# Optimization experiments

Measured on AMD Instinct MI355X. Metric: run time of the kernel, lower is better.

The kernel has to match this reference:

```python
import jax, jax.numpy as jnp
import numpy as np

B, D, V, S = 256, 784, 128, 2  # batch, dim, max_val, n_steps
ITER_PER_CYCLE = 10
STEP_SIZES = [0.5] + [0.1] * (ITER_PER_CYCLE - 1)   # sbc: [big_step] + [small_step]*...
BAL_CONSTS = [0.9] + [0.6] * (ITER_PER_CYCLE - 1)   # sbc: [big_bal] + [small_bal]*...
TEMP = 1.0


def setup_inputs() -> dict:
    key = jax.random.key(0)
    k1, k2, k3, k4, k5 = jax.random.split(key, 5)
    x = jax.random.randint(k1, (B, D), 0, V, dtype=jnp.int32)
    W = jax.random.normal(k2, (D, D), dtype=jnp.float32) * (1.0 / D)  # keep energies moderate
    b = jax.random.normal(k3, (D,), dtype=jnp.float32) * 0.1
    # Pre-sampled Gumbel noise for the categorical proposal (one slab per inner step)
    ug = jax.random.uniform(k4, (S, B, D, V), dtype=jnp.float32, minval=1e-6, maxval=1.0 - 1e-6)
    gumbel = -jnp.log(-jnp.log(ug))
    # Uniform draws for the MH accept/reject test
    u = jax.random.uniform(k5, (S, B), dtype=jnp.float32)
    k_iter = 0
    return {"x": x, "W": W, "b": b, "gumbel": gumbel, "u": u, "k_iter": k_iter}


def reference(x, W, b, gumbel, u, k_iter):
    step_size = STEP_SIZES[k_iter % ITER_PER_CYCLE]
    bal = BAL_CONSTS[k_iter % ITER_PER_CYCLE]
    Wsym = 0.5 * (W + W.T)

    def model(xf):                      # energy: [B]
        return 0.5 * jnp.einsum('bi,bi->b', xf, xf @ Wsym) + xf @ b

    def gradf(xf):                      # d(energy)/dx: [B, D]
        return xf @ Wsym + b

    disc = jnp.arange(V, dtype=jnp.float32)[None, None, :]  # [1,1,V]

    def calc_logits(xf, g):
        # term1 - term2 from _calc_logits, fused elementwise over [B, D, V]
        diff = disc - xf[:, :, None]
        return g[:, :, None] * diff * bal - diff * diff * (0.5 / step_size)

    def body(x_cur, inp):
        g_noise, ui = inp
        xf = x_cur.astype(jnp.float32)
        g = gradf(xf)
        logits = calc_logits(xf, g)                                  # [B,D,V]
        x_delta = jnp.argmax(logits + g_noise, axis=-1)              # categorical sample [B,D]
        logp = jax.nn.log_softmax(logits, axis=-1)
        lp_forward = jnp.take_along_axis(logp, x_delta[:, :, None], axis=-1)[..., 0].sum(axis=1)
        xdf = x_delta.astype(jnp.float32)
        gd = gradf(xdf) / TEMP
        logits_d = calc_logits(xdf, gd)
        logp_d = jax.nn.log_softmax(logits_d, axis=-1)
        lp_reverse = jnp.take_along_axis(logp_d, x_cur[:, :, None], axis=-1)[..., 0].sum(axis=1)
        la = model(xdf) - model(xf) + lp_reverse - lp_forward        # log accept ratio [B]
        acc = jnp.exp(la) > ui
        x_new = jnp.where(acc[:, None], x_delta, x_cur).astype(x_cur.dtype)
        return x_new, la

    x_out, las = jax.lax.scan(body, x, (gumbel, u))
    return x_out, las[-1]
```

## Files before the change

kernel.cpp:

```cpp
#include <hip/hip_runtime.h>

#define B_ 256
#define D_ 784
#define V_ 128
#define S_ 2
#define BD (B_ * D_)
#define KSPLIT 8

__device__ __forceinline__ void get_params(const int* kiter, float& ss, float& bal) {
    int k = kiter[0] % 10;
    ss  = (k == 0) ? 0.5f : 0.1f;
    bal = (k == 0) ? 0.9f : 0.6f;
}

__device__ __forceinline__ double wave_red(double v) {
#pragma unroll
    for (int o = 32; o > 0; o >>= 1) v += __shfl_down(v, o, 64);
    return v;
}

__global__ __launch_bounds__(256) void init_k(
    const float* __restrict__ W, const int* __restrict__ x,
    float* __restrict__ wsym, int* __restrict__ x_cur, float* __restrict__ xf)
{
    int gid = blockIdx.x * 256 + threadIdx.x;
    if (gid < D_ * D_) {
        int i = gid / D_, j = gid % D_;
        wsym[gid] = 0.5f * (W[gid] + W[j * D_ + i]);
    }
    if (gid < BD) {
        int xi = x[gid];
        x_cur[gid] = xi;
        xf[gid] = (float)xi;
    }
}

__global__ __launch_bounds__(256) void gemm_splitk(
    const float* __restrict__ A, const float* __restrict__ Wm,
    float* __restrict__ Cp)
{
    const int bt = blockIdx.x, dt = blockIdx.y, kz = blockIdx.z;
    const int tid = threadIdx.x;
    const int k0 = kz * 98, kend = k0 + 98;

    __shared__ float As[64][17];
    __shared__ float Ws[16][65];

    const int tx = tid & 15, ty = tid >> 4;
    const int arow = tid >> 2, ac0 = (tid & 3) * 4;
    const int wrow = tid >> 4, wc0 = (tid & 15) * 4;

    float acc[4][4] = {};

    for (int kb = k0; kb < kend; kb += 16) {
#pragma unroll
        for (int c = 0; c < 4; ++c) {
            int k = kb + ac0 + c;
            As[arow][ac0 + c] = (k < kend) ? A[(bt * 64 + arow) * D_ + k] : 0.f;
        }
#pragma unroll
        for (int c = 0; c < 4; ++c) {
            int k = kb + wrow;
            int d = dt * 64 + wc0 + c;
            Ws[wrow][wc0 + c] = (k < kend && d < D_) ? Wm[k * D_ + d] : 0.f;
        }
        __syncthreads();
#pragma unroll
        for (int kk = 0; kk < 16; ++kk) {
            float a[4], w[4];
#pragma unroll
            for (int i = 0; i < 4; ++i) a[i] = As[ty * 4 + i][kk];
#pragma unroll
            for (int j = 0; j < 4; ++j) w[j] = Ws[kk][tx * 4 + j];
#pragma unroll
            for (int i = 0; i < 4; ++i)
#pragma unroll
                for (int j = 0; j < 4; ++j)
                    acc[i][j] = fmaf(a[i], w[j], acc[i][j]);
        }
        __syncthreads();
    }

#pragma unroll
    for (int i = 0; i < 4; ++i) {
        int bb = bt * 64 + ty * 4 + i;
#pragma unroll
        for (int j = 0; j < 4; ++j) {
            int d = dt * 64 + tx * 4 + j;
            if (d < D_) Cp[(size_t)kz * BD + (size_t)bb * D_ + d] = acc[i][j];
        }
    }
}

__global__ __launch_bounds__(1024) void forward_k(
    const int* __restrict__ x_cur, const float* __restrict__ gpart,
    const float* __restrict__ bvec, const float* __restrict__ gumbel,
    const int* __restrict__ kiter, int s,
    int* __restrict__ x_delta, float* __restrict__ xdf,
    float* __restrict__ g_out, double* __restrict__ lpf, double* __restrict__ Exf)
{
    const int b = blockIdx.x, tid = threadIdx.x;
    float ss, bal; get_params(kiter, ss, bal);
    const float c2 = 0.5f / ss;

    double lp_acc = 0.0, e_acc = 0.0;

    if (tid < D_) {
        const int d = tid;
        const int bd = b * D_ + d;
        const int xi = x_cur[bd];
        const float xf = (float)xi;

        float gv = 0.f;
#pragma unroll
        for (int p = 0; p < KSPLIT; ++p) gv += gpart[(size_t)p * BD + bd];
        gv += bvec[d];
        g_out[bd] = gv;

        const float a1 = bal * gv;
        const float v0 = xf + a1 * ss;
        int vm = (int)rintf(v0);
        vm = min(127, max(0, vm));
        const float dmv = v0 - (float)vm;
        const float Reff = sqrtf(41.0f / c2 + dmv * dmv);
        int lo = max(0, (int)ceilf(v0 - Reff));
        int hi = min(127, (int)floorf(v0 + Reff));
        lo = min(lo, vm); hi = max(hi, vm);

        const float dvm = (float)vm - xf;
        const float mL = dvm * fmaf(-c2, dvm, a1);
        const float* __restrict__ grow = gumbel + (((size_t)s * B_ + b) * D_ + d) * V_;

        float best = -1e30f; int imax = lo; float sum = 0.f;
        for (int v = lo; v <= hi; ++v) {
            float dv = (float)v - xf;
            float lg = dv * fmaf(-c2, dv, a1);
            float y = lg + grow[v];
            if (y > best) { best = y; imax = v; }
            sum += expf(lg - mL);
        }
        float lse = mL + logf(sum);
        float dvc = (float)imax - xf;
        float lch = dvc * fmaf(-c2, dvc, a1);
        lp_acc = (double)(lch - lse);
        e_acc  = (double)xf * ((double)gv + (double)bvec[d]);
        x_delta[bd] = imax;
        xdf[bd] = (float)imax;
    }

    __shared__ double wred[16];
    const int lane = tid & 63, wv = tid >> 6;
    double t = wave_red(lp_acc);
    if (lane == 0) wred[wv] = t;
    __syncthreads();
    if (tid == 0) { double sm = 0; for (int i = 0; i < 16; ++i) sm += wred[i]; lpf[b] = sm; }
    __syncthreads();
    t = wave_red(e_acc);
    if (lane == 0) wred[wv] = t;
    __syncthreads();
    if (tid == 0) { double sm = 0; for (int i = 0; i < 16; ++i) sm += wred[i]; Exf[b] = sm; }
}

__global__ __launch_bounds__(1024) void reverse_k(
    int* __restrict__ x_cur, const int* __restrict__ x_delta,
    const float* __restrict__ gpart, const float* __restrict__ bvec,
    const float* __restrict__ u, const int* __restrict__ kiter,
    int s, int last, const double* __restrict__ lpf, const double* __restrict__ Exf,
    float* __restrict__ xf_f, float* __restrict__ out)
{
    const int b = blockIdx.x, tid = threadIdx.x;
    float ss, bal; get_params(kiter, ss, bal);
    const float c2 = 0.5f / ss;

    double lp_acc = 0.0, e_acc = 0.0;

    if (tid < D_) {
        const int d = tid;
        const int bd = b * D_ + d;
        const int xi = x_cur[bd];
        const int xd = x_delta[bd];
        const float xdf = (float)xd;

        float gv = 0.f;
#pragma unroll
        for (int p = 0; p < KSPLIT; ++p) gv += gpart[(size_t)p * BD + bd];
        gv += bvec[d];

        const float a1 = bal * gv;
        const float v0 = xdf + a1 * ss;
        int vm = (int)rintf(v0);
        vm = min(127, max(0, vm));
        const float dmv = v0 - (float)vm;
        const float Reff = sqrtf(41.0f / c2 + dmv * dmv);
        int lo = max(0, (int)ceilf(v0 - Reff));
        int hi = min(127, (int)floorf(v0 + Reff));
        lo = min(lo, vm); hi = max(hi, vm);

        const float dvm = (float)vm - xdf;
        const float mL = dvm * fmaf(-c2, dvm, a1);
        float sum = 0.f;
        for (int v = lo; v <= hi; ++v) {
            float dv = (float)v - xdf;
            float lg = dv * fmaf(-c2, dv, a1);
            sum += expf(lg - mL);
        }
        float lse = mL + logf(sum);
        float dvc = (float)xi - xdf;
        float lch = dvc * fmaf(-c2, dvc, a1);
        lp_acc = (double)(lch - lse);
        e_acc  = (double)xdf * ((double)gv + (double)bvec[d]);
    }

    __shared__ double wred[16];
    __shared__ int accept_s;
    __shared__ float la_s;
    const int lane = tid & 63, wv = tid >> 6;

    double t = wave_red(lp_acc);
    if (lane == 0) wred[wv] = t;
    __syncthreads();
    double lpr = 0;
    if (tid == 0) { for (int i = 0; i < 16; ++i) lpr += wred[i]; }
    __syncthreads();
    t = wave_red(e_acc);
    if (lane == 0) wred[wv] = t;
    __syncthreads();
    if (tid == 0) {
        double exd = 0; for (int i = 0; i < 16; ++i) exd += wred[i];
        double la = 0.5 * (exd - Exf[b]) + lpr - lpf[b];
        accept_s = (exp(la) > (double)u[s * B_ + b]) ? 1 : 0;
        la_s = (float)la;
    }
    __syncthreads();

    const int acc = accept_s;
    if (tid < D_) {
        const int bd = b * D_ + tid;
        int xn = acc ? x_delta[bd] : x_cur[bd];
        x_cur[bd] = xn;
        xf_f[bd] = (float)xn;
        if (last) out[bd] = (float)xn;
    }
    if (last && tid == 0) out[BD + b] = la_s;
}

extern "C" void kernel_launch(void* const* d_in, const int* in_sizes, int n_in,
                              void* d_out, int out_size, void* d_ws, size_t ws_size,
                              hipStream_t stream)
{
    const int*   x     = (const int*)d_in[0];
    const float* W     = (const float*)d_in[1];
    const float* bv    = (const float*)d_in[2];
    const float* gum   = (const float*)d_in[3];
    const float* u     = (const float*)d_in[4];
    const int*   kiter = (const int*)d_in[5];
    float* out = (float*)d_out;

    char* w = (char*)d_ws;
    size_t off = 0;
    auto carve = [&](size_t bytes) { void* p = w + off; off += (bytes + 511) & ~511ull; return p; };
    float*  wsym    = (float*)carve((size_t)D_ * D_ * 4);
    int*    x_cur   = (int*)  carve((size_t)BD * 4);
    int*    x_delta = (int*)  carve((size_t)BD * 4);
    float*  xf      = (float*)carve((size_t)BD * 4);
    float*  xdf     = (float*)carve((size_t)BD * 4);
    float*  g       = (float*)carve((size_t)BD * 4);
    float*  gpart   = (float*)carve((size_t)KSPLIT * BD * 4);
    double* lpf     = (double*)carve(B_ * 8);
    double* Exf     = (double*)carve(B_ * 8);
    (void)ws_size; (void)in_sizes; (void)n_in; (void)out_size;

    init_k<<<(D_ * D_ + 255) / 256, 256, 0, stream>>>(W, x, wsym, x_cur, xf);

    for (int s = 0; s < S_; ++s) {
        gemm_splitk<<<dim3(4, 13, KSPLIT), 256, 0, stream>>>(xf, wsym, gpart);
        forward_k<<<B_, 1024, 0, stream>>>(x_cur, gpart, bv, gum, kiter, s,
                                           x_delta, xdf, g, lpf, Exf);
        gemm_splitk<<<dim3(4, 13, KSPLIT), 256, 0, stream>>>(xdf, wsym, gpart);
        reverse_k<<<B_, 1024, 0, stream>>>(x_cur, x_delta, gpart, bv, u, kiter, s,
                                           (s == S_ - 1) ? 1 : 0, lpf, Exf, xf, out);
    }
}
```

Measured before the change: 399.5 us.

## Fuse all stages into one cooperative persistent kernel with grid syncs

Replaces the init, split-K GEMM, forward and reverse kernel launches with a single cooperative kernel of 256 blocks. Grid-wide barriers separate the stages, and per-batch reductions now stay in shared memory. The GEMM is re-tiled as 16 batch rows by a 49-wide K chunk per block, giving 16 partial buffers, with each thread computing one output column directly from global W. This removes eight launch gaps and the lpf/Exf global round-trips. In exchange the GEMM has less reuse per block, the final reduction reads twice as many partials, and grid.sync has its own cost.

New measurement: 1.425 ms. +256.7%, slower.

```diff
diff --git a/kernel.cpp b/kernel.cpp
--- a/kernel.cpp
+++ b/kernel.cpp
@@ -1,17 +1,15 @@
 #include <hip/hip_runtime.h>
+#include <hip/hip_cooperative_groups.h>
+
+namespace cg = cooperative_groups;
 
 #define B_ 256
 #define D_ 784
 #define V_ 128
 #define S_ 2
 #define BD (B_ * D_)
-#define KSPLIT 8
-
-__device__ __forceinline__ void get_params(const int* kiter, float& ss, float& bal) {
-    int k = kiter[0] % 10;
-    ss  = (k == 0) ? 0.5f : 0.1f;
-    bal = (k == 0) ? 0.9f : 0.6f;
-}
+#define KS 16
+#define KC 49
 
 __device__ __forceinline__ double wave_red(double v) {
 #pragma unroll
@@ -19,229 +17,206 @@
     return v;
 }
 
-__global__ __launch_bounds__(256) void init_k(
-    const float* __restrict__ W, const int* __restrict__ x,
-    float* __restrict__ wsym, int* __restrict__ x_cur, float* __restrict__ xf)
+__global__ __launch_bounds__(1024, 4) void mega_k(
+    const int* __restrict__ x, const float* __restrict__ W,
+    const float* __restrict__ bv, const float* __restrict__ gum,
+    const float* __restrict__ u, const int* __restrict__ kiter,
+    float* __restrict__ wsym, int* __restrict__ x_cur,
+    int* __restrict__ x_delta, float* __restrict__ xf,
+    float* __restrict__ xdf, float* __restrict__ gpart,
+    float* __restrict__ out)
 {
-    int gid = blockIdx.x * 256 + threadIdx.x;
-    if (gid < D_ * D_) {
+    cg::grid_group grid = cg::this_grid();
+    const int tid = threadIdx.x;
+    const int blk = blockIdx.x;
+    const int gstride = 256 * 1024;
+
+    __shared__ float As[16][KC];
+    __shared__ double wred[16];
+    __shared__ double lpf_s, Exf_s;
+    __shared__ int acc_s;
+    __shared__ float la_s;
+
+    for (int gid = blk * 1024 + tid; gid < D_ * D_; gid += gstride) {
         int i = gid / D_, j = gid % D_;
         wsym[gid] = 0.5f * (W[gid] + W[j * D_ + i]);
     }
-    if (gid < BD) {
+    for (int gid = blk * 1024 + tid; gid < BD; gid += gstride) {
         int xi = x[gid];
         x_cur[gid] = xi;
         xf[gid] = (float)xi;
     }
-}
-
-__global__ __launch_bounds__(256) void gemm_splitk(
-    const float* __restrict__ A, const float* __restrict__ Wm,
-    float* __restrict__ Cp)
-{
-    const int bt = blockIdx.x, dt = blockIdx.y, kz = blockIdx.z;
-    const int tid = threadIdx.x;
-    const int k0 = kz * 98, kend = k0 + 98;
-
-    __shared__ float As[64][17];
-    __shared__ float Ws[16][65];
-
-    const int tx = tid & 15, ty = tid >> 4;
-    const int arow = tid >> 2, ac0 = (tid & 3) * 4;
-    const int wrow = tid >> 4, wc0 = (tid & 15) * 4;
-
-    float acc[4][4] = {};
-
-    for (int kb = k0; kb < kend; kb += 16) {
-#pragma unroll
-        for (int c = 0; c < 4; ++c) {
-            int k = kb + ac0 + c;
-            As[arow][ac0 + c] = (k < kend) ? A[(bt * 64 + arow) * D_ + k] : 0.f;
-        }
-#pragma unroll
-        for (int c = 0; c < 4; ++c) {
-            int k = kb + wrow;
-            int d = dt * 64 + wc0 + c;
-            Ws[wrow][wc0 + c] = (k < kend && d < D_) ? Wm[k * D_ + d] : 0.f;
-        }
-        __syncthreads();
-#pragma unroll
-        for (int kk = 0; kk < 16; ++kk) {
-            float a[4], w[4];
-#pragma unroll
-            for (int i = 0; i < 4; ++i) a[i] = As[ty * 4 + i][kk];
-#pragma unroll
-            for (int j = 0; j < 4; ++j) w[j] = Ws[kk][tx * 4 + j];
-#pragma unroll
-            for (int i = 0; i < 4; ++i)
-#pragma unroll
-                for (int j = 0; j < 4; ++j)
-                    acc[i][j] = fmaf(a[i], w[j], acc[i][j]);
-        }
-        __syncthreads();
+    const int kmod = kiter[0] % 10;
+    const float ss  = (kmod == 0) ? 0.5f : 0.1f;
+    const float bal = (kmod == 0) ? 0.9f : 0.6f;
+    const float c2 = 0.5f / ss;
+
+    const int bt = blk >> 4, kz = blk & 15;
+    const int k0 = kz * KC;
+    const int lane = tid & 63, wv = tid >> 6;
+
+    __threadfence();
+    grid.sync();
+
+    for (int s = 0; s < S_; ++s) {
+        {
+            for (int idx = tid; idx < 16 * KC; idx += 1024) {
+                int r = idx / KC, c = idx % KC;
+                As[r][c] = xf[(bt * 16 + r) * D_ + k0 + c];
+            }
+            __syncthreads();
+            if (tid < D_) {
+                float acc[16] = {};
+                for (int kk = 0; kk < KC; ++kk) {
+                    float wval = wsym[(k0 + kk) * D_ + tid];
+#pragma unroll
+                    for (int i = 0; i < 16; ++i)
+                        acc[i] = fmaf(As[i][kk], wval, acc[i]);
+                }
+#pragma unroll
+                for (int i = 0; i < 16; ++i)
+                    gpart[(size_t)kz * BD + (size_t)(bt * 16 + i) * D_ + tid] = acc[i];
+            }
+        }
+        __threadfence();
+        grid.sync();
+
+        {
+            const int b = blk;
+            double lp_acc = 0.0, e_acc = 0.0;
+            if (tid < D_) {
+                const int d = tid, bd = b * D_ + d;
+                const int xi = x_cur[bd];
+                const float xfv = (float)xi;
+                float gv = 0.f;
+#pragma unroll
+                for (int p = 0; p < KS; ++p) gv += gpart[(size_t)p * BD + bd];
+                gv += bv[d];
+                const float a1 = bal * gv;
+                const float v0 = xfv + a1 * ss;
+                int vm = (int)rintf(v0); vm = min(127, max(0, vm));
+                const float dmv = v0 - (float)vm;
+                const float Reff = sqrtf(41.0f / c2 + dmv * dmv);
+                int lo = max(0, (int)ceilf(v0 - Reff));
+                int hi = min(127, (int)floorf(v0 + Reff));
+                lo = min(lo, vm); hi = max(hi, vm);
+                const float dvm = (float)vm - xfv;
+                const float mL = dvm * fmaf(-c2, dvm, a1);
+                const float* __restrict__ grow = gum + (((size_t)s * B_ + b) * D_ + d) * V_;
+                float best = -1e30f; int imax = lo; float sum = 0.f;
+                for (int v = lo; v <= hi; ++v) {
+                    float dv = (float)v - xfv;
+                    float lg = dv * fmaf(-c2, dv, a1);
+                    float y = lg + grow[v];
+                    if (y > best) { best = y; imax = v; }
+                    sum += expf(lg - mL);
+                }
+                float lse = mL + logf(sum);
+                float dvc = (float)imax - xfv;
+                float lch = dvc * fmaf(-c2, dvc, a1);
+                lp_acc = (double)(lch - lse);
+                e_acc  = (double)xfv * ((double)gv + (double)bv[d]);
+                x_delta[bd] = imax;
+                xdf[bd] = (float)imax;
+            }
+            double t = wave_red(lp_acc);
+            if (lane == 0) wred[wv] = t;
+            __syncthreads();
+            if (tid == 0) { double sm = 0; for (int i = 0; i < 16; ++i) sm += wred[i]; lpf_s = sm; }
+            __syncthreads();
+            t = wave_red(e_acc);
+            if (lane == 0) wred[wv] = t;
+            __syncthreads();
+            if (tid == 0) { double sm = 0; for (int i = 0; i < 16; ++i) sm += wred[i]; Exf_s = sm; }
+        }
+        __threadfence();
+        grid.sync();
+
+        {
+            for (int idx = tid; idx < 16 * KC; idx += 1024) {
+                int r = idx / KC, c = idx % KC;
+                As[r][c] = xdf[(bt * 16 + r) * D_ + k0 + c];
+            }
+            __syncthreads();
+            if (tid < D_) {
+                float acc[16] = {};
+                for (int kk = 0; kk < KC; ++kk) {
+                    float wval = wsym[(k0 + kk) * D_ + tid];
+#pragma unroll
+                    for (int i = 0; i < 16; ++i)
+                        acc[i] = fmaf(As[i][kk], wval, acc[i]);
+                }
+#pragma unroll
+                for (int i = 0; i < 16; ++i)
+                    gpart[(size_t)kz * BD + (size_t)(bt * 16 + i) * D_ + tid] = acc[i];
+            }
+        }
+        __threadfence();
+        grid.sync();
+
+        {
+            const int b = blk;
+            double lp_acc = 0.0, e_acc = 0.0;
+            if (tid < D_) {
+                const int d = tid, bd = b * D_ + d;
+                const int xi = x_cur[bd];
+                const int xd = x_delta[bd];
+                const float xdv = (float)xd;
+                float gv = 0.f;
+#pragma unroll
+                for (int p = 0; p < KS; ++p) gv += gpart[(size_t)p * BD + bd];
+                gv += bv[d];
+                const float a1 = bal * gv;
+                const float v0 = xdv + a1 * ss;
+                int vm = (int)rintf(v0); vm = min(127, max(0, vm));
+                const float dmv = v0 - (float)vm;
+                const float Reff = sqrtf(41.0f / c2 + dmv * dmv);
+                int lo = max(0, (int)ceilf(v0 - Reff));
+                int hi = min(127, (int)floorf(v0 + Reff));
+                lo = min(lo, vm); hi = max(hi, vm);
+                const float dvm = (float)vm - xdv;
+                const float mL = dvm * fmaf(-c2, dvm, a1);
+                float sum = 0.f;
+                for (int v = lo; v <= hi; ++v) {
+                    float dv = (float)v - xdv;
+                    float lg = dv * fmaf(-c2, dv, a1);
+                    sum += expf(lg - mL);
+                }
+                float lse = mL + logf(sum);
+                float dvc = (float)xi - xdv;
+                float lch = dvc * fmaf(-c2, dvc, a1);
+                lp_acc = (double)(lch - lse);
+                e_acc  = (double)xdv * ((double)gv + (double)bv[d]);
+            }
+            double t = wave_red(lp_acc);
+            if (lane == 0) wred[wv] = t;
+            __syncthreads();
+            double lpr = 0;
+            if (tid == 0) { for (int i = 0; i < 16; ++i) lpr += wred[i]; }
+            __syncthreads();
+            t = wave_red(e_acc);
+            if (lane == 0) wred[wv] = t;
+            __syncthreads();
+            if (tid == 0) {
+                double exd = 0; for (int i = 0; i < 16; ++i) exd += wred[i];
+                double la = 0.5 * (exd - Exf_s) + lpr - lpf_s;
+                acc_s = (exp(la) > (double)u[s * B_ + b]) ? 1 : 0;
+                la_s = (float)la;
+            }
+            __syncthreads();
+            const int acc = acc_s;
+            if (tid < D_) {
+                const int bd = b * D_ + tid;
+                int xn = acc ? x_delta[bd] : x_cur[bd];
+                x_cur[bd] = xn;
+                xf[bd] = (float)xn;
+                if (s == S_ - 1) out[bd] = (float)xn;
+            }
+            if (s == S_ - 1 && tid == 0) out[BD + b] = la_s;
+        }
+        __threadfence();
+        grid.sync();
     }
-
-#pragma unroll
-    for (int i = 0; i < 4; ++i) {
-        int bb = bt * 64 + ty * 4 + i;
-#pragma unroll
-        for (int j = 0; j < 4; ++j) {
-            int d = dt * 64 + tx * 4 + j;
-            if (d < D_) Cp[(size_t)kz * BD + (size_t)bb * D_ + d] = acc[i][j];
-        }
-    }
-}
-
-__global__ __launch_bounds__(1024) void forward_k(
-    const int* __restrict__ x_cur, const float* __restrict__ gpart,
-    const float* __restrict__ bvec, const float* __restrict__ gumbel,
-    const int* __restrict__ kiter, int s,
-    int* __restrict__ x_delta, float* __restrict__ xdf,
-    float* __restrict__ g_out, double* __restrict__ lpf, double* __restrict__ Exf)
-{
-    const int b = blockIdx.x, tid = threadIdx.x;
-    float ss, bal; get_params(kiter, ss, bal);
-    const float c2 = 0.5f / ss;
-
-    double lp_acc = 0.0, e_acc = 0.0;
-
-    if (tid < D_) {
-        const int d = tid;
-        const int bd = b * D_ + d;
-        const int xi = x_cur[bd];
-        const float xf = (float)xi;
-
-        float gv = 0.f;
-#pragma unroll
-        for (int p = 0; p < KSPLIT; ++p) gv += gpart[(size_t)p * BD + bd];
-        gv += bvec[d];
-        g_out[bd] = gv;
-
-        const float a1 = bal * gv;
-        const float v0 = xf + a1 * ss;
-        int vm = (int)rintf(v0);
-        vm = min(127, max(0, vm));
-        const float dmv = v0 - (float)vm;
-        const float Reff = sqrtf(41.0f / c2 + dmv * dmv);
-        int lo = max(0, (int)ceilf(v0 - Reff));
-        int hi = min(127, (int)floorf(v0 + Reff));
-        lo = min(lo, vm); hi = max(hi, vm);
-
-        const float dvm = (float)vm - xf;
-        const float mL = dvm * fmaf(-c2, dvm, a1);
-        const float* __restrict__ grow = gumbel + (((size_t)s * B_ + b) * D_ + d) * V_;
-
-        float best = -1e30f; int imax = lo; float sum = 0.f;
-        for (int v = lo; v <= hi; ++v) {
-            float dv = (float)v - xf;
-            float lg = dv * fmaf(-c2, dv, a1);
-            float y = lg + grow[v];
-            if (y > best) { best = y; imax = v; }
-            sum += expf(lg - mL);
-        }
-        float lse = mL + logf(sum);
-        float dvc = (float)imax - xf;
-        float lch = dvc * fmaf(-c2, dvc, a1);
-        lp_acc = (double)(lch - lse);
-        e_acc  = (double)xf * ((double)gv + (double)bvec[d]);
-        x_delta[bd] = imax;
-        xdf[bd] = (float)imax;
-    }
-
-    __shared__ double wred[16];
-    const int lane = tid & 63, wv = tid >> 6;
-    double t = wave_red(lp_acc);
-    if (lane == 0) wred[wv] = t;
-    __syncthreads();
-    if (tid == 0) { double sm = 0; for (int i = 0; i < 16; ++i) sm += wred[i]; lpf[b] = sm; }
-    __syncthreads();
-    t = wave_red(e_acc);
-    if (lane == 0) wred[wv] = t;
-    __syncthreads();
-    if (tid == 0) { double sm = 0; for (int i = 0; i < 16; ++i) sm += wred[i]; Exf[b] = sm; }
-}
-
-__global__ __launch_bounds__(1024) void reverse_k(
-    int* __restrict__ x_cur, const int* __restrict__ x_delta,
-    const float* __restrict__ gpart, const float* __restrict__ bvec,
-    const float* __restrict__ u, const int* __restrict__ kiter,
-    int s, int last, const double* __restrict__ lpf, const double* __restrict__ Exf,
-    float* __restrict__ xf_f, float* __restrict__ out)
-{
-    const int b = blockIdx.x, tid = threadIdx.x;
-    float ss, bal; get_params(kiter, ss, bal);
-    const float c2 = 0.5f / ss;
-
-    double lp_acc = 0.0, e_acc = 0.0;
-
-    if (tid < D_) {
-        const int d = tid;
-        const int bd = b * D_ + d;
-        const int xi = x_cur[bd];
-        const int xd = x_delta[bd];
-        const float xdf = (float)xd;
-
-        float gv = 0.f;
-#pragma unroll
-        for (int p = 0; p < KSPLIT; ++p) gv += gpart[(size_t)p * BD + bd];
-        gv += bvec[d];
-
-        const float a1 = bal * gv;
-        const float v0 = xdf + a1 * ss;
-        int vm = (int)rintf(v0);
-        vm = min(127, max(0, vm));
-        const float dmv = v0 - (float)vm;
-        const float Reff = sqrtf(41.0f / c2 + dmv * dmv);
-        int lo = max(0, (int)ceilf(v0 - Reff));
-        int hi = min(127, (int)floorf(v0 + Reff));
-        lo = min(lo, vm); hi = max(hi, vm);
-
-        const float dvm = (float)vm - xdf;
-        const float mL = dvm * fmaf(-c2, dvm, a1);
-        float sum = 0.f;
-        for (int v = lo; v <= hi; ++v) {
-            float dv = (float)v - xdf;
-            float lg = dv * fmaf(-c2, dv, a1);
-            sum += expf(lg - mL);
-        }
-        float lse = mL + logf(sum);
-        float dvc = (float)xi - xdf;
-        float lch = dvc * fmaf(-c2, dvc, a1);
-        lp_acc = (double)(lch - lse);
-        e_acc  = (double)xdf * ((double)gv + (double)bvec[d]);
-    }
-
-    __shared__ double wred[16];
-    __shared__ int accept_s;
-    __shared__ float la_s;
-    const int lane = tid & 63, wv = tid >> 6;
-
-    double t = wave_red(lp_acc);
-    if (lane == 0) wred[wv] = t;
-    __syncthreads();
-    double lpr = 0;
-    if (tid == 0) { for (int i = 0; i < 16; ++i) lpr += wred[i]; }
-    __syncthreads();
-    t = wave_red(e_acc);
-    if (lane == 0) wred[wv] = t;
-    __syncthreads();
-    if (tid == 0) {
-        double exd = 0; for (int i = 0; i < 16; ++i) exd += wred[i];
-        double la = 0.5 * (exd - Exf[b]) + lpr - lpf[b];
-        accept_s = (exp(la) > (double)u[s * B_ + b]) ? 1 : 0;
-        la_s = (float)la;
-    }
-    __syncthreads();
-
-    const int acc = accept_s;
-    if (tid < D_) {
-        const int bd = b * D_ + tid;
-        int xn = acc ? x_delta[bd] : x_cur[bd];
-        x_cur[bd] = xn;
-        xf_f[bd] = (float)xn;
-        if (last) out[bd] = (float)xn;
-    }
-    if (last && tid == 0) out[BD + b] = la_s;
 }
 
 extern "C" void kernel_launch(void* const* d_in, const int* in_sizes, int n_in,
@@ -259,25 +234,19 @@
     char* w = (char*)d_ws;
     size_t off = 0;
     auto carve = [&](size_t bytes) { void* p = w + off; off += (bytes + 511) & ~511ull; return p; };
-    float*  wsym    = (float*)carve((size_t)D_ * D_ * 4);
-    int*    x_cur   = (int*)  carve((size_t)BD * 4);
-    int*    x_delta = (int*)  carve((size_t)BD * 4);
-    float*  xf      = (float*)carve((size_t)BD * 4);
-    float*  xdf     = (float*)carve((size_t)BD * 4);
-    float*  g       = (float*)carve((size_t)BD * 4);
-    float*  gpart   = (float*)carve((size_t)KSPLIT * BD * 4);
-    double* lpf     = (double*)carve(B_ * 8);
-    double* Exf     = (double*)carve(B_ * 8);
+    float* wsym    = (float*)carve((size_t)D_ * D_ * 4);
+    int*   x_cur   = (int*)  carve((size_t)BD * 4);
+    int*   x_delta = (int*)  carve((size_t)BD * 4);
+    float* xf      = (float*)carve((size_t)BD * 4);
+    float* xdf     = (float*)carve((size_t)BD * 4);
+    float* gpart   = (float*)carve((size_t)KS * BD * 4);
     (void)ws_size; (void)in_sizes; (void)n_in; (void)out_size;
 
-    init_k<<<(D_ * D_ + 255) / 256, 256, 0, stream>>>(W, x, wsym, x_cur, xf);
-
-    for (int s = 0; s < S_; ++s) {
-        gemm_splitk<<<dim3(4, 13, KSPLIT), 256, 0, stream>>>(xf, wsym, gpart);
-        forward_k<<<B_, 1024, 0, stream>>>(x_cur, gpart, bv, gum, kiter, s,
-                                           x_delta, xdf, g, lpf, Exf);
-        gemm_splitk<<<dim3(4, 13, KSPLIT), 256, 0, stream>>>(xdf, wsym, gpart);
-        reverse_k<<<B_, 1024, 0, stream>>>(x_cur, x_delta, gpart, bv, u, kiter, s,
-                                           (s == S_ - 1) ? 1 : 0, lpf, Exf, xf, out);
-    }
+    void* args[] = {
+        (void*)&x, (void*)&W, (void*)&bv, (void*)&gum, (void*)&u, (void*)&kiter,
+        (void*)&wsym, (void*)&x_cur, (void*)&x_delta, (void*)&xf, (void*)&xdf,
+        (void*)&gpart, (void*)&out
+    };
+    hipLaunchCooperativeKernel((const void*)mega_k, dim3(256), dim3(1024),
+                               args, 0, stream);
 }
```
